# Kernel tuning notes

Hardware: AMD Instinct MI355X
Metric: run time of the kernel (lower is better)

The kernel has to match this reference:

```python
import jax, jax.numpy as jnp
import numpy as np
import math

IMG_COUNT = 5      # total_length = id_length + 1
NUM_TOKENS = 576   # (768//32)**2, the is_1024_resolution branch
CHANNELS = 1280
N_SEL = 288        # sa32 * NUM_TOKENS
HEADS = 20


def setup_inputs() -> dict:
    key = jax.random.key(0)
    ks = jax.random.split(key, 7)
    hidden_states = jax.random.normal(ks[0], (2 * IMG_COUNT, NUM_TOKENS, CHANNELS), dtype=jnp.float32)
    scale = 0.02
    Wq = jax.random.normal(ks[1], (CHANNELS, CHANNELS), dtype=jnp.float32) * scale
    Wk = jax.random.normal(ks[2], (CHANNELS, CHANNELS), dtype=jnp.float32) * scale
    Wv = jax.random.normal(ks[3], (CHANNELS, CHANNELS), dtype=jnp.float32) * scale
    Wo = jax.random.normal(ks[4], (CHANNELS, CHANNELS), dtype=jnp.float32) * scale
    bo = jnp.zeros((CHANNELS,), dtype=jnp.float32)
    # per-image random spatial token subsets (cal_attn_indice_xl_effcient_memory)
    indices = jax.random.randint(ks[5], (IMG_COUNT, N_SEL), 0, NUM_TOKENS, dtype=jnp.int64)
    return {"hidden_states": hidden_states, "Wq": Wq, "Wk": Wk, "Wv": Wv,
            "Wo": Wo, "bo": bo, "indices": indices, "heads": HEADS}


def _sdpa_block(q_in, kv_in, Wq, Wk, Wv, Wo, bo, heads):
    """Faithful __call2__: linear q/k/v, multi-head SDPA, output projection."""
    B, Tq, C = q_in.shape
    Tk = kv_in.shape[1]
    hd = C // heads
    q = (q_in @ Wq.T).reshape(B, Tq, heads, hd).transpose(0, 2, 1, 3)   # [B,H,Tq,hd]
    k = (kv_in @ Wk.T).reshape(B, Tk, heads, hd).transpose(0, 2, 1, 3)  # [B,H,Tk,hd]
    v = (kv_in @ Wv.T).reshape(B, Tk, heads, hd).transpose(0, 2, 1, 3)
    scale = 1.0 / math.sqrt(hd)
    scores = jnp.einsum('bhqd,bhkd->bhqk', q, k) * scale
    probs = jax.nn.softmax(scores, axis=-1)
    o = jnp.einsum('bhqk,bhkd->bhqd', probs, v)
    o = o.transpose(0, 2, 1, 3).reshape(B, Tq, C)
    return o @ Wo.T + bo


def reference(hidden_states, Wq, Wk, Wv, Wo, bo, indices, heads):
    B, T, C = hidden_states.shape
    P = indices.shape[0]          # img_count
    hs = hidden_states.reshape(2, P, T, C)
    # gathered[p] = hs[:, p, indices[p], :] -> [2, P, n_sel, C]
    gathered = hs[:, jnp.arange(P)[:, None], indices, :]
    outs = []
    for i in range(P):            # small fixed loop over images (structurally distinct KV banks)
        cur = hs[:, i]            # [2, T, C]
        others = jnp.concatenate([gathered[:, p] for p in range(P) if p != i], axis=1)
        enc = jnp.concatenate([others, cur], axis=1)  # [2, (P-1)*n_sel + T, C]
        outs.append(_sdpa_block(cur, enc, Wq, Wk, Wv, Wo, bo, heads))
    return jnp.stack(outs, axis=1).reshape(B, T, C)
```

## Files before the change

### kernel.cpp

```cpp
#include <hip/hip_runtime.h>

typedef __bf16 bf16_t;
typedef __attribute__((ext_vector_type(4))) __bf16 bf16x4;
typedef __attribute__((ext_vector_type(8))) __bf16 bf16x8;
typedef __attribute__((ext_vector_type(4))) float f32x4;

#define MFMA_BF16(a, b, c) __builtin_amdgcn_mfma_f32_16x16x32_bf16((a), (b), (c), 0, 0, 0)

namespace {

constexpr int PIMG  = 5;
constexpr int TTOK  = 576;
constexpr int CCH   = 1280;
constexpr int NSEL  = 288;
constexpr int NH    = 20;
constexpr int ROWS  = 2 * PIMG * TTOK;
constexpr int TKEYS = 4 * NSEL + TTOK;
constexpr int KT_TILES = TKEYS / 64;
constexpr size_t NXE = (size_t)ROWS * CCH;
constexpr size_t NWE = (size_t)CCH * CCH;

__device__ __forceinline__ bf16x8 cvt8(const float* p) {
  const float4 f0 = *(const float4*)p;
  const float4 f1 = *(const float4*)(p + 4);
  bf16x8 r;
  r[0] = (bf16_t)f0.x; r[1] = (bf16_t)f0.y; r[2] = (bf16_t)f0.z; r[3] = (bf16_t)f0.w;
  r[4] = (bf16_t)f1.x; r[5] = (bf16_t)f1.y; r[6] = (bf16_t)f1.z; r[7] = (bf16_t)f1.w;
  return r;
}

__device__ __forceinline__ void gload_lds16(const bf16_t* g, bf16_t* l) {
  __builtin_amdgcn_global_load_lds((const __attribute__((address_space(1))) void*)g,
                                   (__attribute__((address_space(3))) void*)l, 16, 0, 0);
}

__global__ __launch_bounds__(256) void cvt_kernel(
    const float* __restrict__ X, const float* __restrict__ W0, const float* __restrict__ W1,
    const float* __restrict__ W2, const float* __restrict__ W3,
    bf16_t* __restrict__ Xb, bf16_t* __restrict__ Wb0, bf16_t* __restrict__ Wb1,
    bf16_t* __restrict__ Wb2, bf16_t* __restrict__ Wb3) {
  const int y = blockIdx.y;
  const float* src = y == 0 ? X : (y == 1 ? W0 : (y == 2 ? W1 : (y == 3 ? W2 : W3)));
  bf16_t* dst = y == 0 ? Xb : (y == 1 ? Wb0 : (y == 2 ? Wb1 : (y == 3 ? Wb2 : Wb3)));
  const size_t n = y == 0 ? NXE : NWE;
  const size_t idx = ((size_t)blockIdx.x * 256 + threadIdx.x) * 8;
  if (idx < n) *(bf16x8*)&dst[idx] = cvt8(&src[idx]);
}

template <bool BIAS, typename CT>
__device__ __forceinline__ void gemm_nt_body(const bf16_t* __restrict__ A,
                                             const bf16_t* __restrict__ B,
                                             const float* __restrict__ bias,
                                             CT* __restrict__ C,
                                             int bm, int bn, float scale) {
  __shared__ bf16_t As[128 * 64];
  __shared__ bf16_t Bs[128 * 64];

  const int tid  = threadIdx.x;
  const int lane = tid & 63;
  const int wave = tid >> 6;
  const int quad = lane >> 4;
  const int l16  = lane & 15;
  const int wr   = (wave >> 1) * 64;
  const int wc   = (wave & 1) * 64;
  const int m0   = bm * 128;
  const int n0   = bn * 128;
  const int lr   = lane >> 3;
  const int lc   = (lane & 7) * 8;

  f32x4 acc[4][4];
#pragma unroll
  for (int i = 0; i < 4; ++i)
#pragma unroll
    for (int j = 0; j < 4; ++j) acc[i][j] = (f32x4){0.f, 0.f, 0.f, 0.f};

  for (int k0 = 0; k0 < CCH; k0 += 64) {
    __syncthreads();
#pragma unroll
    for (int p = 0; p < 4; ++p) {
      const int rb = 32 * wave + 8 * p;
      gload_lds16(&A[(size_t)(m0 + rb + lr) * CCH + k0 + lc], &As[rb * 64 + lane * 8]);
      gload_lds16(&B[(size_t)(n0 + rb + lr) * CCH + k0 + lc], &Bs[rb * 64 + lane * 8]);
    }
    __syncthreads();

#pragma unroll
    for (int ks = 0; ks < 2; ++ks) {
      bf16x8 af[4], bfr[4];
#pragma unroll
      for (int i = 0; i < 4; ++i)
        af[i] = *(const bf16x8*)&As[(wr + 16 * i + l16) * 64 + ks * 32 + quad * 8];
#pragma unroll
      for (int j = 0; j < 4; ++j)
        bfr[j] = *(const bf16x8*)&Bs[(wc + 16 * j + l16) * 64 + ks * 32 + quad * 8];
#pragma unroll
      for (int i = 0; i < 4; ++i)
#pragma unroll
        for (int j = 0; j < 4; ++j)
          acc[i][j] = MFMA_BF16(af[i], bfr[j], acc[i][j]);
    }
  }

#pragma unroll
  for (int j = 0; j < 4; ++j) {
    const int col = n0 + wc + 16 * j + l16;
    const float bv = BIAS ? bias[col] : 0.f;
#pragma unroll
    for (int i = 0; i < 4; ++i) {
#pragma unroll
      for (int r = 0; r < 4; ++r) {
        const int row = m0 + wr + 16 * i + quad * 4 + r;
        const float val = acc[i][j][r] * scale + bv;
        if constexpr (sizeof(CT) == 2)
          C[(size_t)row * CCH + col] = (CT)val;
        else
          C[(size_t)row * CCH + col] = val;
      }
    }
  }
}

__global__ __launch_bounds__(256, 4) void qkv_gemm_kernel(
    const bf16_t* __restrict__ Xb,
    const bf16_t* __restrict__ Wqb, const bf16_t* __restrict__ Wkb, const bf16_t* __restrict__ Wvb,
    bf16_t* __restrict__ Qf, bf16_t* __restrict__ Kf, bf16_t* __restrict__ Vf) {
  const bf16_t* W = blockIdx.z == 0 ? Wqb : (blockIdx.z == 1 ? Wkb : Wvb);
  bf16_t* O = blockIdx.z == 0 ? Qf : (blockIdx.z == 1 ? Kf : Vf);
  const float scl = blockIdx.z == 0 ? 0.125f : 1.0f;
  gemm_nt_body<false, bf16_t>(Xb, W, nullptr, O, blockIdx.x, blockIdx.y, scl);
}

__global__ __launch_bounds__(256, 4) void out_gemm_kernel(
    const bf16_t* __restrict__ Of, const bf16_t* __restrict__ Wob,
    const float* __restrict__ bo, float* __restrict__ out) {
  gemm_nt_body<true, float>(Of, Wob, bo, out, blockIdx.x, blockIdx.y, 1.0f);
}

__global__ __launch_bounds__(256, 4) void attn_kernel(
    const bf16_t* __restrict__ Qf, const bf16_t* __restrict__ Kf, const bf16_t* __restrict__ Vf,
    const int* __restrict__ indices, bf16_t* __restrict__ Ofull) {
  __shared__ int kvrow[TKEYS];
  __shared__ bf16_t Ks[64 * 72];
  __shared__ bf16_t Vts[64 * 64];
  __shared__ bf16_t Ps[64 * 72];
  __shared__ float lred[64 * 16];
  __shared__ float linv[64];

  const int tid  = threadIdx.x;
  const int lane = tid & 63;
  const int wave = tid >> 6;
  const int quad = lane >> 4;
  const int l16  = lane & 15;
  const int qt   = blockIdx.x;
  const int h    = blockIdx.y;
  const int si   = blockIdx.z;
  const int s    = si / PIMG;
  const int ii   = si % PIMG;

  const int r0 = si * TTOK + qt * 64;
  const int hc = h * 64;

  bf16x8 aq[4][2];
#pragma unroll
  for (int n = 0; n < 4; ++n)
#pragma unroll
    for (int h2 = 0; h2 < 2; ++h2)
      aq[n][h2] = *(const bf16x8*)&Qf[(size_t)(r0 + 16 * n + l16) * CCH + hc + quad * 8 + 32 * h2];

  for (int j = tid; j < TKEYS; j += 256) {
    int row;
    if (j < 4 * NSEL) {
      const int jp = j / NSEL;
      const int jj = j - jp * NSEL;
      const int p  = jp + (jp >= ii ? 1 : 0);
      row = (s * PIMG + p) * TTOK + indices[p * NSEL + jj];
    } else {
      row = si * TTOK + (j - 4 * NSEL);
    }
    kvrow[j] = row;
  }
  __syncthreads();

  const int jrow = tid >> 3;
  const int cdim = (tid & 7) * 8;
  bf16x8 kvv[2], vvv[2];
  auto prefetch = [&](int kt) {
    const int ra = kvrow[kt * 64 + jrow];
    const int rb = kvrow[kt * 64 + jrow + 32];
    kvv[0] = *(const bf16x8*)&Kf[(size_t)ra * CCH + hc + cdim];
    kvv[1] = *(const bf16x8*)&Kf[(size_t)rb * CCH + hc + cdim];
    vvv[0] = *(const bf16x8*)&Vf[(size_t)ra * CCH + hc + cdim];
    vvv[1] = *(const bf16x8*)&Vf[(size_t)rb * CCH + hc + cdim];
  };
  prefetch(0);

  float l_part[4] = {0.f, 0.f, 0.f, 0.f};
  f32x4 oacc[4];
#pragma unroll
  for (int n = 0; n < 4; ++n) oacc[n] = (f32x4){0.f, 0.f, 0.f, 0.f};

  for (int kt = 0; kt < KT_TILES; ++kt) {
    *(bf16x8*)&Ks[jrow * 72 + cdim] = kvv[0];
    *(bf16x8*)&Ks[(jrow + 32) * 72 + cdim] = kvv[1];
    const int cb0 = jrow ^ cdim;
    const int cb1 = (jrow + 32) ^ cdim;
#pragma unroll
    for (int x = 0; x < 8; ++x) {
      Vts[(cdim + x) * 64 + cb0] = vvv[0][x];
      Vts[(cdim + x) * 64 + cb1] = vvv[1][x];
    }
    __syncthreads();
    if (kt < KT_TILES - 1) prefetch(kt + 1);

    const bf16x8 kf0 = *(const bf16x8*)&Ks[(16 * wave + l16) * 72 + quad * 8];
    const bf16x8 kf1 = *(const bf16x8*)&Ks[(16 * wave + l16) * 72 + quad * 8 + 32];
    f32x4 sacc[4];
#pragma unroll
    for (int n = 0; n < 4; ++n) {
      f32x4 z = (f32x4){0.f, 0.f, 0.f, 0.f};
      z = MFMA_BF16(kf0, aq[n][0], z);
      z = MFMA_BF16(kf1, aq[n][1], z);
      sacc[n] = z;
    }

#pragma unroll
    for (int n = 0; n < 4; ++n) {
      bf16x4 pb;
      float sum = 0.f;
#pragma unroll
      for (int r = 0; r < 4; ++r) {
        const float pv = __expf(sacc[n][r]);
        pb[r] = (bf16_t)pv;
        sum += pv;
      }
      l_part[n] += sum;
      *(bf16x4*)&Ps[(16 * n + l16) * 72 + 16 * wave + 4 * quad] = pb;
    }
    __syncthreads();

    const bf16x8 vf0 = *(const bf16x8*)&Vts[(16 * wave + l16) * 64 + ((quad * 8) ^ ((16 * wave + l16) & 56))];
    const bf16x8 vf1 = *(const bf16x8*)&Vts[(16 * wave + l16) * 64 + ((quad * 8 + 32) ^ ((16 * wave + l16) & 56))];
#pragma unroll
    for (int n = 0; n < 4; ++n) {
      const bf16x8 pf0 = *(const bf16x8*)&Ps[(16 * n + l16) * 72 + quad * 8];
      const bf16x8 pf1 = *(const bf16x8*)&Ps[(16 * n + l16) * 72 + quad * 8 + 32];
      oacc[n] = MFMA_BF16(pf0, vf0, oacc[n]);
      oacc[n] = MFMA_BF16(pf1, vf1, oacc[n]);
    }
    __syncthreads();
  }

#pragma unroll
  for (int n = 0; n < 4; ++n)
    lred[(16 * n + l16) * 16 + 4 * wave + quad] = l_part[n];
  __syncthreads();
  if (tid < 64) {
    float t = 0.f;
#pragma unroll
    for (int i = 0; i < 16; ++i) t += lred[tid * 16 + i];
    linv[tid] = 1.f / t;
  }
  __syncthreads();
#pragma unroll
  for (int n = 0; n < 4; ++n) {
    const f32x4 lv = *(const f32x4*)&linv[16 * n + 4 * quad];
#pragma unroll
    for (int r = 0; r < 4; ++r) {
      const int qloc = 16 * n + 4 * quad + r;
      Ofull[(size_t)(r0 + qloc) * CCH + hc + 16 * wave + l16] = (bf16_t)(oacc[n][r] * lv[r]);
    }
  }
}

}

extern "C" void kernel_launch(void* const* d_in, const int* in_sizes, int n_in,
                              void* d_out, int out_size, void* d_ws, size_t ws_size,
                              hipStream_t stream) {
  const float* hs = (const float*)d_in[0];
  const float* Wq = (const float*)d_in[1];
  const float* Wk = (const float*)d_in[2];
  const float* Wv = (const float*)d_in[3];
  const float* Wo = (const float*)d_in[4];
  const float* bo = (const float*)d_in[5];
  const int* indices = (const int*)d_in[6];
  float* out = (float*)d_out;

  bf16_t* Qf  = (bf16_t*)d_ws;
  bf16_t* Kf  = Qf + NXE;
  bf16_t* Vf  = Kf + NXE;
  bf16_t* Xb  = Vf + NXE;
  bf16_t* Of  = Xb;
  bf16_t* Wqb = Xb + NXE;
  bf16_t* Wkb = Wqb + NWE;
  bf16_t* Wvb = Wkb + NWE;
  bf16_t* Wob = Wvb + NWE;

  dim3 g0((NXE + 2047) / 2048, 5);
  cvt_kernel<<<g0, dim3(256), 0, stream>>>(hs, Wq, Wk, Wv, Wo, Xb, Wqb, Wkb, Wvb, Wob);

  dim3 g1(ROWS / 128, CCH / 128, 3);
  qkv_gemm_kernel<<<g1, dim3(256), 0, stream>>>(Xb, Wqb, Wkb, Wvb, Qf, Kf, Vf);

  dim3 g2(TTOK / 64, NH, 2 * PIMG);
  attn_kernel<<<g2, dim3(256), 0, stream>>>(Qf, Kf, Vf, indices, Of);

  dim3 g3(ROWS / 128, CCH / 128, 1);
  out_gemm_kernel<<<g3, dim3(256), 0, stream>>>(Of, Wob, bo, out);
}
```

Before: 330.0 us.

## Register-prefetch GEMM tiles with padded LDS and remap attention blocks per XCD

The GEMM body drops direct global-to-LDS loads and instead prefetches the next K tile into registers while the current one is consumed, writing it into LDS rows padded to 72 to cut bank conflicts. GEMM occupancy hints go from 4 to 3. The attention kernel now uses a 1D grid swizzled so each XCD gets all query tiles of the same (image, head) pair, aiming for better L2 reuse of K/V. Its LDS use shrinks through 16-bit kv row indices and reuse of the K/V buffers for the reduction scratch, with an occupancy hint of 5. The trade-offs are higher register pressure from the prefetch and reliance on row indices fitting in 16 bits.

```diff
diff --git a/kernel.cpp b/kernel.cpp
--- a/kernel.cpp
+++ b/kernel.cpp
@@ -27,11 +27,6 @@
   r[0] = (bf16_t)f0.x; r[1] = (bf16_t)f0.y; r[2] = (bf16_t)f0.z; r[3] = (bf16_t)f0.w;
   r[4] = (bf16_t)f1.x; r[5] = (bf16_t)f1.y; r[6] = (bf16_t)f1.z; r[7] = (bf16_t)f1.w;
   return r;
-}
-
-__device__ __forceinline__ void gload_lds16(const bf16_t* g, bf16_t* l) {
-  __builtin_amdgcn_global_load_lds((const __attribute__((address_space(1))) void*)g,
-                                   (__attribute__((address_space(3))) void*)l, 16, 0, 0);
 }
 
 __global__ __launch_bounds__(256) void cvt_kernel(
@@ -53,8 +48,9 @@
                                              const float* __restrict__ bias,
                                              CT* __restrict__ C,
                                              int bm, int bn, float scale) {
-  __shared__ bf16_t As[128 * 64];
-  __shared__ bf16_t Bs[128 * 64];
+  constexpr int LDT = 72;
+  __shared__ bf16_t As[128 * LDT];
+  __shared__ bf16_t Bs[128 * LDT];
 
   const int tid  = threadIdx.x;
   const int lane = tid & 63;
@@ -65,8 +61,18 @@
   const int wc   = (wave & 1) * 64;
   const int m0   = bm * 128;
   const int n0   = bn * 128;
-  const int lr   = lane >> 3;
-  const int lc   = (lane & 7) * 8;
+  const int srow = tid >> 3;
+  const int scol = (tid & 7) * 8;
+
+  bf16x8 pa[4], pb[4];
+  auto loadAB = [&](int k0) {
+#pragma unroll
+    for (int p = 0; p < 4; ++p) {
+      pa[p] = *(const bf16x8*)&A[(size_t)(m0 + srow + 32 * p) * CCH + k0 + scol];
+      pb[p] = *(const bf16x8*)&B[(size_t)(n0 + srow + 32 * p) * CCH + k0 + scol];
+    }
+  };
+  loadAB(0);
 
   f32x4 acc[4][4];
 #pragma unroll
@@ -74,31 +80,30 @@
 #pragma unroll
     for (int j = 0; j < 4; ++j) acc[i][j] = (f32x4){0.f, 0.f, 0.f, 0.f};
 
-  for (int k0 = 0; k0 < CCH; k0 += 64) {
+  for (int it = 0; it < CCH / 64; ++it) {
+#pragma unroll
+    for (int p = 0; p < 4; ++p) {
+      *(bf16x8*)&As[(srow + 32 * p) * LDT + scol] = pa[p];
+      *(bf16x8*)&Bs[(srow + 32 * p) * LDT + scol] = pb[p];
+    }
     __syncthreads();
-#pragma unroll
-    for (int p = 0; p < 4; ++p) {
-      const int rb = 32 * wave + 8 * p;
-      gload_lds16(&A[(size_t)(m0 + rb + lr) * CCH + k0 + lc], &As[rb * 64 + lane * 8]);
-      gload_lds16(&B[(size_t)(n0 + rb + lr) * CCH + k0 + lc], &Bs[rb * 64 + lane * 8]);
-    }
-    __syncthreads();
-
+    if (it < CCH / 64 - 1) loadAB((it + 1) * 64);
 #pragma unroll
     for (int ks = 0; ks < 2; ++ks) {
       bf16x8 af[4], bfr[4];
 #pragma unroll
       for (int i = 0; i < 4; ++i)
-        af[i] = *(const bf16x8*)&As[(wr + 16 * i + l16) * 64 + ks * 32 + quad * 8];
+        af[i] = *(const bf16x8*)&As[(wr + 16 * i + l16) * LDT + ks * 32 + quad * 8];
 #pragma unroll
       for (int j = 0; j < 4; ++j)
-        bfr[j] = *(const bf16x8*)&Bs[(wc + 16 * j + l16) * 64 + ks * 32 + quad * 8];
+        bfr[j] = *(const bf16x8*)&Bs[(wc + 16 * j + l16) * LDT + ks * 32 + quad * 8];
 #pragma unroll
       for (int i = 0; i < 4; ++i)
 #pragma unroll
         for (int j = 0; j < 4; ++j)
           acc[i][j] = MFMA_BF16(af[i], bfr[j], acc[i][j]);
     }
+    if (it < CCH / 64 - 1) __syncthreads();
   }
 
 #pragma unroll
@@ -120,7 +125,7 @@
   }
 }
 
-__global__ __launch_bounds__(256, 4) void qkv_gemm_kernel(
+__global__ __launch_bounds__(256, 3) void qkv_gemm_kernel(
     const bf16_t* __restrict__ Xb,
     const bf16_t* __restrict__ Wqb, const bf16_t* __restrict__ Wkb, const bf16_t* __restrict__ Wvb,
     bf16_t* __restrict__ Qf, bf16_t* __restrict__ Kf, bf16_t* __restrict__ Vf) {
@@ -130,32 +135,36 @@
   gemm_nt_body<false, bf16_t>(Xb, W, nullptr, O, blockIdx.x, blockIdx.y, scl);
 }
 
-__global__ __launch_bounds__(256, 4) void out_gemm_kernel(
+__global__ __launch_bounds__(256, 3) void out_gemm_kernel(
     const bf16_t* __restrict__ Of, const bf16_t* __restrict__ Wob,
     const float* __restrict__ bo, float* __restrict__ out) {
   gemm_nt_body<true, float>(Of, Wob, bo, out, blockIdx.x, blockIdx.y, 1.0f);
 }
 
-__global__ __launch_bounds__(256, 4) void attn_kernel(
+__global__ __launch_bounds__(256, 5) void attn_kernel(
     const bf16_t* __restrict__ Qf, const bf16_t* __restrict__ Kf, const bf16_t* __restrict__ Vf,
     const int* __restrict__ indices, bf16_t* __restrict__ Ofull) {
-  __shared__ int kvrow[TKEYS];
+  __shared__ unsigned short kvrow[TKEYS];
   __shared__ bf16_t Ks[64 * 72];
   __shared__ bf16_t Vts[64 * 64];
   __shared__ bf16_t Ps[64 * 72];
-  __shared__ float lred[64 * 16];
-  __shared__ float linv[64];
 
   const int tid  = threadIdx.x;
   const int lane = tid & 63;
   const int wave = tid >> 6;
   const int quad = lane >> 4;
   const int l16  = lane & 15;
-  const int qt   = blockIdx.x;
-  const int h    = blockIdx.y;
-  const int si   = blockIdx.z;
-  const int s    = si / PIMG;
-  const int ii   = si % PIMG;
+
+  const int b   = blockIdx.x;
+  const int xcd = b & 7;
+  const int t   = b >> 3;
+  const int gi  = t / 9;
+  const int qt  = t - gi * 9;
+  const int g   = xcd + 8 * gi;
+  const int h   = g % NH;
+  const int si  = g / NH;
+  const int s   = si / PIMG;
+  const int ii  = si % PIMG;
 
   const int r0 = si * TTOK + qt * 64;
   const int hc = h * 64;
@@ -177,7 +186,7 @@
     } else {
       row = si * TTOK + (j - 4 * NSEL);
     }
-    kvrow[j] = row;
+    kvrow[j] = (unsigned short)row;
   }
   __syncthreads();
 
@@ -250,24 +259,26 @@
     __syncthreads();
   }
 
+  float* lred = (float*)Ks;
+  float* linv = (float*)Vts;
 #pragma unroll
   for (int n = 0; n < 4; ++n)
     lred[(16 * n + l16) * 16 + 4 * wave + quad] = l_part[n];
   __syncthreads();
   if (tid < 64) {
-    float t = 0.f;
-#pragma unroll
-    for (int i = 0; i < 16; ++i) t += lred[tid * 16 + i];
-    linv[tid] = 1.f / t;
+    float tt = 0.f;
+#pragma unroll
+    for (int i = 0; i < 16; ++i) tt += lred[tid * 16 + i];
+    linv[tid] = 1.f / tt;
   }
   __syncthreads();
 #pragma unroll
   for (int n = 0; n < 4; ++n) {
-    const f32x4 lv = *(const f32x4*)&linv[16 * n + 4 * quad];
 #pragma unroll
     for (int r = 0; r < 4; ++r) {
       const int qloc = 16 * n + 4 * quad + r;
-      Ofull[(size_t)(r0 + qloc) * CCH + hc + 16 * wave + l16] = (bf16_t)(oacc[n][r] * lv[r]);
+      Ofull[(size_t)(r0 + qloc) * CCH + hc + 16 * wave + l16] =
+          (bf16_t)(oacc[n][r] * linv[qloc]);
     }
   }
 }
@@ -302,8 +313,7 @@
   dim3 g1(ROWS / 128, CCH / 128, 3);
   qkv_gemm_kernel<<<g1, dim3(256), 0, stream>>>(Xb, Wqb, Wkb, Wvb, Qf, Kf, Vf);
 
-  dim3 g2(TTOK / 64, NH, 2 * PIMG);
-  attn_kernel<<<g2, dim3(256), 0, stream>>>(Qf, Kf, Vf, indices, Of);
+  attn_kernel<<<dim3(1800), dim3(256), 0, stream>>>(Qf, Kf, Vf, indices, Of);
 
   dim3 g3(ROWS / 128, CCH / 128, 1);
   out_gemm_kernel<<<g3, dim3(256), 0, stream>>>(Of, Wob, bo, out);
```

Result: slower. 371.1 us (+12.5%).
